# Optimization experiments

Hardware: AMD Instinct MI355X
Metric: run time of the kernel (lower is better)

The kernel has to match this reference:

```python
import jax, jax.numpy as jnp
import numpy as np

NNODES = 8192
K = 512
NEG_SLOPE = 0.01  # torch F.leaky_relu default
EPS = 1e-12       # torch F.normalize default eps


def setup_inputs() -> dict:
    key = jax.random.key(0)
    kx, kp = jax.random.split(key)
    x = jax.random.normal(kx, (NNODES, K), dtype=jnp.float32)
    # xavier_uniform init for proto (nnodes, k)
    bound = float(np.sqrt(6.0 / (NNODES + K)))
    proto = jax.random.uniform(kp, (NNODES, K), dtype=jnp.float32,
                               minval=-bound, maxval=bound)
    return {"x": x, "proto": proto}


def reference(x, proto):
    # In-place no_grad step in torch: proto <- l2norm(proto), rows unit-norm.
    norm = jnp.sqrt(jnp.sum(proto * proto, axis=1, keepdims=True))
    pn = proto / jnp.maximum(norm, EPS)  # (nnodes, k), unit rows
    # cosine_similarity over all pairs == pn @ pn.T since rows are unit-norm.
    # This fuses torch's (nnodes, nnodes, k) broadcast into one GEMM.
    sim = jnp.einsum('ik,jk->ij', pn, pn)  # (nnodes, nnodes)
    return jnp.where(sim >= 0, sim, NEG_SLOPE * sim)
```

## Files before the change

### kernel.cpp

```cpp
#include <hip/hip_runtime.h>
#include <stdint.h>

#define NN 8192
#define KD 512
#define BM 128
#define BK 32
#define NTILE (NN / BM)
#define NTRI (NTILE * (NTILE + 1) / 2)
#define NKT (KD / BK)

typedef __bf16 bf16;
typedef __bf16 bf16x8 __attribute__((ext_vector_type(8)));
typedef float f32x4 __attribute__((ext_vector_type(4)));

__global__ __launch_bounds__(256) void rownorm_kernel(const float* __restrict__ proto,
                                                      bf16* __restrict__ pn) {
    const int row  = blockIdx.x * 4 + (threadIdx.x >> 6);
    const int lane = threadIdx.x & 63;
    const float4* src = (const float4*)(proto + (size_t)row * KD) + lane * 2;
    const float4 v0 = src[0];
    const float4 v1 = src[1];
    float s = v0.x*v0.x + v0.y*v0.y + v0.z*v0.z + v0.w*v0.w
            + v1.x*v1.x + v1.y*v1.y + v1.z*v1.z + v1.w*v1.w;
#pragma unroll
    for (int off = 32; off; off >>= 1) s += __shfl_xor(s, off);
    const float inv = 1.0f / fmaxf(sqrtf(s), 1e-12f);
    bf16x8 o;
    o[0] = (bf16)(v0.x*inv); o[1] = (bf16)(v0.y*inv);
    o[2] = (bf16)(v0.z*inv); o[3] = (bf16)(v0.w*inv);
    o[4] = (bf16)(v1.x*inv); o[5] = (bf16)(v1.y*inv);
    o[6] = (bf16)(v1.z*inv); o[7] = (bf16)(v1.w*inv);
    *(bf16x8*)(pn + (size_t)row * KD + lane * 8) = o;
}

__device__ __forceinline__ void gload_lds16(const bf16* g, bf16* l) {
    __builtin_amdgcn_global_load_lds(
        (const __attribute__((address_space(1))) void*)g,
        (__attribute__((address_space(3))) void*)l, 16, 0, 0);
}

__device__ __forceinline__ float lrelu(float v) {
    return (v >= 0.0f) ? v : 0.01f * v;
}

__global__ __launch_bounds__(256, 4) void gemm_sym_kernel(const bf16* __restrict__ P,
                                                          float* __restrict__ C) {
    __shared__ bf16 sA[2][BM][BK];
    __shared__ bf16 sB[2][BM][BK];

    const int bid = blockIdx.x;
    const int swz = (bid & 7) * (NTRI / 8) + (bid >> 3);
    int tm = 0, rem = swz;
    while (rem >= NTILE - tm) { rem -= NTILE - tm; ++tm; }
    const int tn = tm + rem;

    const int tid  = threadIdx.x;
    const int w    = tid >> 6;
    const int lane = tid & 63;
    const int rowA0 = tm * BM;
    const int rowB0 = tn * BM;
    const int wm = (w >> 1) * 64;
    const int wn = (w & 1) * 64;
    const int rsel  = lane & 15;
    const int khalf = (lane >> 4) * 8;

    const int chunk0 = w * 128 + lane;
    const bf16* g0 = P + (size_t)(chunk0 >> 2) * KD + (chunk0 & 3) * 8;
    const size_t offA = (size_t)rowA0 * KD;
    const size_t offB = (size_t)rowB0 * KD;
    const int ldsOff0 = w * 1024;
    const int ldsOff1 = w * 1024 + 512;

    f32x4 acc[4][4] = {};

#define STAGE(buf, kt)                                                  \
    do {                                                                \
        gload_lds16(g0 + offA + (kt),           &sA[buf][0][0] + ldsOff0); \
        gload_lds16(g0 + offA + 16 * KD + (kt), &sA[buf][0][0] + ldsOff1); \
        gload_lds16(g0 + offB + (kt),           &sB[buf][0][0] + ldsOff0); \
        gload_lds16(g0 + offB + 16 * KD + (kt), &sB[buf][0][0] + ldsOff1); \
    } while (0)

#define COMPUTE(buf)                                                        \
    do {                                                                    \
        bf16x8 af[4], bfr[4];                                               \
        _Pragma("unroll")                                                   \
        for (int m = 0; m < 4; ++m)                                         \
            af[m] = *(const bf16x8*)&sA[buf][wm + m * 16 + rsel][khalf];    \
        _Pragma("unroll")                                                   \
        for (int n = 0; n < 4; ++n)                                         \
            bfr[n] = *(const bf16x8*)&sB[buf][wn + n * 16 + rsel][khalf];   \
        _Pragma("unroll")                                                   \
        for (int m = 0; m < 4; ++m)                                         \
            _Pragma("unroll")                                               \
            for (int n = 0; n < 4; ++n)                                     \
                acc[m][n] = __builtin_amdgcn_mfma_f32_16x16x32_bf16(        \
                    af[m], bfr[n], acc[m][n], 0, 0, 0);                     \
    } while (0)

    STAGE(0, 0);
    __syncthreads();

#pragma unroll
    for (int t = 0; t < NKT; ++t) {
        if (t < NKT - 1) STAGE((t + 1) & 1, (t + 1) * BK);
        COMPUTE(t & 1);
        if (t < NKT - 1) __syncthreads();
    }

    const int cr = (lane >> 4) * 4;
    const int cc = lane & 15;

#pragma unroll
    for (int m = 0; m < 4; ++m)
#pragma unroll
        for (int n = 0; n < 4; ++n)
#pragma unroll
            for (int r = 0; r < 4; ++r)
                C[(size_t)(rowA0 + wm + m * 16 + cr + r) * NN
                  + (rowB0 + wn + n * 16 + cc)] = lrelu(acc[m][n][r]);

    if (tm != tn) {
#pragma unroll
        for (int m = 0; m < 4; ++m)
#pragma unroll
            for (int n = 0; n < 4; ++n) {
                float4 vv;
                vv.x = lrelu(acc[m][n][0]);
                vv.y = lrelu(acc[m][n][1]);
                vv.z = lrelu(acc[m][n][2]);
                vv.w = lrelu(acc[m][n][3]);
                *(float4*)&C[(size_t)(rowB0 + wn + n * 16 + cc) * NN
                             + (rowA0 + wm + m * 16 + cr)] = vv;
            }
    }
#undef STAGE
#undef COMPUTE
}

extern "C" void kernel_launch(void* const* d_in, const int* in_sizes, int n_in,
                              void* d_out, int out_size, void* d_ws, size_t ws_size,
                              hipStream_t stream) {
    const float* proto = (const float*)d_in[1];
    float* C  = (float*)d_out;
    bf16* pn  = (bf16*)d_ws;

    rownorm_kernel<<<dim3(NN / 4), dim3(256), 0, stream>>>(proto, pn);
    gemm_sym_kernel<<<dim3(NTRI), dim3(256), 0, stream>>>(pn, C);
}
```

Before: 101.7 us.

## Stage GEMM epilogue through LDS for coalesced direct and transposed stores

The accumulator tile is written to a padded shared-memory buffer, one 64-row half at a time. It is then read back so that each row of the direct output and of the mirrored (transposed) output goes out as contiguous float4 stores. This replaces the previous scattered scalar stores and strided transposed float4 stores, aiming to improve write coalescing on the large output matrix, which dominates traffic. In exchange it adds extra barriers, LDS round-trips and a slightly larger shared allocation that aliases the operand buffers. The padded stride of 129 floats also makes the float4 LDS reads unaligned.

```diff
diff --git a/kernel.cpp b/kernel.cpp
--- a/kernel.cpp
+++ b/kernel.cpp
@@ -45,8 +45,10 @@
 
 __global__ __launch_bounds__(256, 4) void gemm_sym_kernel(const bf16* __restrict__ P,
                                                           float* __restrict__ C) {
-    __shared__ bf16 sA[2][BM][BK];
-    __shared__ bf16 sB[2][BM][BK];
+    __shared__ __align__(16) unsigned char smem[33024];
+    bf16*  sA = (bf16*)smem;
+    bf16*  sB = (bf16*)(smem + 16384);
+    float* sE = (float*)smem;
 
     const int bid = blockIdx.x;
     const int swz = (bid & 7) * (NTRI / 8) + (bid >> 3);
@@ -57,12 +59,13 @@
     const int tid  = threadIdx.x;
     const int w    = tid >> 6;
     const int lane = tid & 63;
+    const int wr = w >> 1;
     const int rowA0 = tm * BM;
     const int rowB0 = tn * BM;
-    const int wm = (w >> 1) * 64;
+    const int wm = wr * 64;
     const int wn = (w & 1) * 64;
-    const int rsel  = lane & 15;
-    const int khalf = (lane >> 4) * 8;
+    const int rr = lane & 15;
+    const int h  = lane >> 4;
 
     const int chunk0 = w * 128 + lane;
     const bf16* g0 = P + (size_t)(chunk0 >> 2) * KD + (chunk0 & 3) * 8;
@@ -73,29 +76,31 @@
 
     f32x4 acc[4][4] = {};
 
-#define STAGE(buf, kt)                                                  \
-    do {                                                                \
-        gload_lds16(g0 + offA + (kt),           &sA[buf][0][0] + ldsOff0); \
-        gload_lds16(g0 + offA + 16 * KD + (kt), &sA[buf][0][0] + ldsOff1); \
-        gload_lds16(g0 + offB + (kt),           &sB[buf][0][0] + ldsOff0); \
-        gload_lds16(g0 + offB + 16 * KD + (kt), &sB[buf][0][0] + ldsOff1); \
+#define STAGE(buf, kt)                                                        \
+    do {                                                                      \
+        gload_lds16(g0 + offA + (kt),           sA + (buf) * 4096 + ldsOff0); \
+        gload_lds16(g0 + offA + 16 * KD + (kt), sA + (buf) * 4096 + ldsOff1); \
+        gload_lds16(g0 + offB + (kt),           sB + (buf) * 4096 + ldsOff0); \
+        gload_lds16(g0 + offB + 16 * KD + (kt), sB + (buf) * 4096 + ldsOff1); \
     } while (0)
 
-#define COMPUTE(buf)                                                        \
-    do {                                                                    \
-        bf16x8 af[4], bfr[4];                                               \
-        _Pragma("unroll")                                                   \
-        for (int m = 0; m < 4; ++m)                                         \
-            af[m] = *(const bf16x8*)&sA[buf][wm + m * 16 + rsel][khalf];    \
-        _Pragma("unroll")                                                   \
-        for (int n = 0; n < 4; ++n)                                         \
-            bfr[n] = *(const bf16x8*)&sB[buf][wn + n * 16 + rsel][khalf];   \
-        _Pragma("unroll")                                                   \
-        for (int m = 0; m < 4; ++m)                                         \
-            _Pragma("unroll")                                               \
-            for (int n = 0; n < 4; ++n)                                     \
-                acc[m][n] = __builtin_amdgcn_mfma_f32_16x16x32_bf16(        \
-                    af[m], bfr[n], acc[m][n], 0, 0, 0);                     \
+#define COMPUTE(buf)                                                          \
+    do {                                                                      \
+        const bf16* ra_ = sA + (buf) * 4096;                                  \
+        const bf16* rb_ = sB + (buf) * 4096;                                  \
+        bf16x8 af[4], bfr[4];                                                 \
+        _Pragma("unroll")                                                     \
+        for (int m = 0; m < 4; ++m)                                           \
+            af[m] = *(const bf16x8*)(ra_ + (wm + m * 16 + rr) * 32 + h * 8);  \
+        _Pragma("unroll")                                                     \
+        for (int n = 0; n < 4; ++n)                                           \
+            bfr[n] = *(const bf16x8*)(rb_ + (wn + n * 16 + rr) * 32 + h * 8); \
+        _Pragma("unroll")                                                     \
+        for (int m = 0; m < 4; ++m)                                           \
+            _Pragma("unroll")                                                 \
+            for (int n = 0; n < 4; ++n)                                       \
+                acc[m][n] = __builtin_amdgcn_mfma_f32_16x16x32_bf16(          \
+                    af[m], bfr[n], acc[m][n], 0, 0, 0);                       \
     } while (0)
 
     STAGE(0, 0);
@@ -108,31 +113,46 @@
         if (t < NKT - 1) __syncthreads();
     }
 
-    const int cr = (lane >> 4) * 4;
-    const int cc = lane & 15;
+    const int cr = h * 4;
+    const int cc = rr;
 
 #pragma unroll
-    for (int m = 0; m < 4; ++m)
+    for (int H = 0; H < 2; ++H) {
+        __syncthreads();
+        if (wr == H) {
 #pragma unroll
-        for (int n = 0; n < 4; ++n)
+            for (int m = 0; m < 4; ++m)
 #pragma unroll
-            for (int r = 0; r < 4; ++r)
-                C[(size_t)(rowA0 + wm + m * 16 + cr + r) * NN
-                  + (rowB0 + wn + n * 16 + cc)] = lrelu(acc[m][n][r]);
+                for (int n = 0; n < 4; ++n)
+#pragma unroll
+                    for (int r = 0; r < 4; ++r)
+                        sE[(m * 16 + cr + r) * 129 + wn + n * 16 + cc] =
+                            lrelu(acc[m][n][r]);
+        }
+        __syncthreads();
 
-    if (tm != tn) {
 #pragma unroll
-        for (int m = 0; m < 4; ++m)
+        for (int k = 0; k < 8; ++k) {
+            const int seg = tid + k * 256;
+            const int lr  = seg >> 5;
+            const int c4  = (seg & 31) * 4;
+            const float4 v = *(const float4*)&sE[lr * 129 + c4];
+            *(float4*)&C[(size_t)(rowA0 + H * 64 + lr) * NN + rowB0 + c4] = v;
+        }
+
+        if (tm != tn) {
 #pragma unroll
-            for (int n = 0; n < 4; ++n) {
-                float4 vv;
-                vv.x = lrelu(acc[m][n][0]);
-                vv.y = lrelu(acc[m][n][1]);
-                vv.z = lrelu(acc[m][n][2]);
-                vv.w = lrelu(acc[m][n][3]);
-                *(float4*)&C[(size_t)(rowB0 + wn + n * 16 + cc) * NN
-                             + (rowA0 + wm + m * 16 + cr)] = vv;
+            for (int rd = 0; rd < 8; ++rd) {
+                const int j = (tid >> 4) + rd * 16;
+                const int i0 = (tid & 15) * 4;
+                float4 v;
+                v.x = sE[(i0 + 0) * 129 + j];
+                v.y = sE[(i0 + 1) * 129 + j];
+                v.z = sE[(i0 + 2) * 129 + j];
+                v.w = sE[(i0 + 3) * 129 + j];
+                *(float4*)&C[(size_t)(rowB0 + j) * NN + rowA0 + H * 64 + i0] = v;
             }
+        }
     }
 #undef STAGE
 #undef COMPUTE
```

Measured after the change: 94.05 us, median of 2. 7.5% less time.
